# Performance work log

Measured on AMD Instinct MI355X. Metric: run time of the kernel, lower is better.

## Reference

```python
import jax, jax.numpy as jnp
import numpy as np

ATOM_F = 64
NBR_F = 64
IN_F = 2 * ATOM_F + NBR_F  # 192
ATTN = ATOM_F              # 64
ATTN_OUT = 4 * ATOM_F      # 256
EPS = 1e-5


def setup_inputs() -> dict:
    key = jax.random.key(0)
    ks = jax.random.split(key, 12)
    N, M = 65536, 12
    atom_in_fea = jax.random.normal(ks[0], (N, ATOM_F), dtype=jnp.float32)
    nbr_fea = jax.random.normal(ks[1], (N, M, NBR_F), dtype=jnp.float32)
    nbr_fea_idx = jax.random.randint(ks[2], (N, M), 0, N)
    s = 0.05
    WK = jax.random.normal(ks[3], (ATTN, IN_F), dtype=jnp.float32) * s
    WQ = jax.random.normal(ks[4], (ATTN, IN_F), dtype=jnp.float32) * s
    WV = jax.random.normal(ks[5], (ATTN, IN_F), dtype=jnp.float32) * s
    WO = jax.random.normal(ks[6], (ATTN_OUT, ATTN), dtype=jnp.float32) * s
    W_fc = jax.random.normal(ks[7], (2 * ATOM_F, ATTN_OUT), dtype=jnp.float32) * s
    b_fc = jax.random.normal(ks[8], (2 * ATOM_F,), dtype=jnp.float32) * s
    bn1_g = jnp.ones((2 * ATOM_F,), jnp.float32)
    bn1_b = jnp.zeros((2 * ATOM_F,), jnp.float32)
    bn2_g = jnp.ones((ATOM_F,), jnp.float32)
    bn2_b = jnp.zeros((ATOM_F,), jnp.float32)
    return {"atom_in_fea": atom_in_fea, "nbr_fea": nbr_fea, "nbr_fea_idx": nbr_fea_idx,
            "WK": WK, "WQ": WQ, "WV": WV, "WO": WO, "W_fc": W_fc, "b_fc": b_fc,
            "bn1_g": bn1_g, "bn1_b": bn1_b, "bn2_g": bn2_g, "bn2_b": bn2_b}


def _batchnorm(x2d, g, b):
    # training-mode BatchNorm1d: biased variance over the batch dim
    mean = jnp.mean(x2d, axis=0)
    var = jnp.mean((x2d - mean) ** 2, axis=0)
    return (x2d - mean) * jax.lax.rsqrt(var + EPS) * g + b


def reference(atom_in_fea, nbr_fea, nbr_fea_idx, WK, WQ, WV, WO,
              W_fc, b_fc, bn1_g, bn1_b, bn2_g, bn2_b):
    N, M = nbr_fea_idx.shape
    atom_nbr_fea = atom_in_fea[nbr_fea_idx]                       # (N, M, F)
    self_fea = jnp.broadcast_to(atom_in_fea[:, None, :], (N, M, ATOM_F))
    total = jnp.concatenate([self_fea, atom_nbr_fea, nbr_fea], axis=2)  # (N, M, 192)

    # self-attention over the M neighbor slots (dropout is identity at eval)
    K = jnp.einsum('nmf,af->nma', total, WK)
    Q = jnp.einsum('nmf,af->nma', total, WQ)
    V = jnp.einsum('nmf,af->nma', total, WV)
    logits = jnp.einsum('nma,nka->nmk', K, Q) / jnp.sqrt(jnp.float32(ATTN))
    w = jax.nn.softmax(logits, axis=-1)
    attn = jnp.einsum('nmk,nka->nma', w, V)                       # (N, M, 64)
    h = jnp.einsum('nma,oa->nmo', attn, WO)                       # (N, M, 256)

    gated = jnp.einsum('nmo,go->nmg', h, W_fc) + b_fc             # (N, M, 128)
    gated = _batchnorm(gated.reshape(-1, 2 * ATOM_F), bn1_g, bn1_b).reshape(N, M, 2 * ATOM_F)
    nbr_filter, nbr_core = jnp.split(gated, 2, axis=2)
    nbr_sumed = jnp.sum(jax.nn.sigmoid(nbr_filter) * jax.nn.softplus(nbr_core), axis=1)  # (N, 64)
    nbr_sumed = _batchnorm(nbr_sumed, bn2_g, bn2_b)
    return jax.nn.softplus(atom_in_fea + nbr_sumed)
```

## Files before the change

kernel.cpp:

```cpp
#include <hip/hip_runtime.h>
#include <stdint.h>


typedef unsigned short u16;
typedef __attribute__((ext_vector_type(8))) short short8;
typedef __attribute__((ext_vector_type(4))) short short4v;
typedef __attribute__((ext_vector_type(4))) float floatx4;

#define EPS 1e-5f
#define LOG2E 1.44269504f

#if defined(__has_builtin)
#if __has_builtin(__builtin_amdgcn_mfma_f32_16x16x16bf16_1k)
#define HAVE_M16 1
#endif
#endif
#ifndef HAVE_M16
#define HAVE_M16 0
#endif

#if HAVE_M16
#define VKW 20
#define WKW 20
#else
#define VKW 40
#define WKW 40
#endif

__device__ __forceinline__ u16 bf16r(float x) {
  uint32_t u = __float_as_uint(x);
  u = (u + 0x7fffu + ((u >> 16) & 1u)) >> 16;
  return (u16)u;
}
__device__ __forceinline__ float bf2f(u16 h) {
  return __uint_as_float(((uint32_t)h) << 16);
}
__device__ __forceinline__ uint32_t pkbf16(float a, float b) {
  union { __bf16 h[2]; uint32_t u; } r;
  r.h[0] = (__bf16)a; r.h[1] = (__bf16)b;
  return r.u;
}
__device__ __forceinline__ short8 pkfrag(float4 a, float4 b) {
  union { uint32_t u[4]; short8 s; } r;
  r.u[0] = pkbf16(a.x, a.y); r.u[1] = pkbf16(a.z, a.w);
  r.u[2] = pkbf16(b.x, b.y); r.u[3] = pkbf16(b.z, b.w);
  return r.s;
}
__device__ __forceinline__ float fexp(float x) { return __builtin_amdgcn_exp2f(x * LOG2E); }
__device__ __forceinline__ float frcp(float x) { return __builtin_amdgcn_rcpf(x); }
__device__ __forceinline__ float fsig(float x) { return frcp(1.0f + fexp(-x)); }
__device__ __forceinline__ float fsp(float x) {
  return fmaxf(x, 0.0f) + __builtin_amdgcn_logf(1.0f + fexp(-fabsf(x))) * 0.69314718f;
}

#define MFMA32(a, b, c) __builtin_amdgcn_mfma_f32_16x16x32_bf16((a), (b), (c), 0, 0, 0)

#define OFF_FRAGE 0
#define OFF_FRAGP 24576
#define OFF_FRAGC 73728
#define OFF_BN1S1 90112
#define OFF_BN1S2 221184
#define OFF_BN2S1 352256
#define OFF_BN2S2 417792
#define OFF_BNST  483328
#define OFF_NSUM  524288
#define OFF_P     17825792
#define OFF_ATTN  68157440

__global__ __launch_bounds__(256) void k_prep(
    const float* __restrict__ WK, const float* __restrict__ WQ, const float* __restrict__ WV,
    const float* __restrict__ WO, const float* __restrict__ Wfc,
    u16* __restrict__ fragE, u16* __restrict__ fragP, u16* __restrict__ fragC,
    float* __restrict__ zbase) {
  int b = blockIdx.x, t = threadIdx.x;
  if (b < 24) {
    int c = b >> 1, ks = b & 1;
    for (int e = t; e < 512; e += 256) {
      int l = e >> 3, j = e & 7;
      int col = c * 16 + (l & 15);
      int k = ks * 32 + ((l >> 4) & 3) * 8 + j;
      int which = col >> 6, a = col & 63;
      const float* W = (which == 0) ? WK : ((which == 1) ? WQ : WV);
      fragE[b * 512 + e] = bf16r(W[a * 192 + 128 + k]);
    }
  } else if (b < 72) {
    int tt = b - 24; int ks = tt & 1; int ct = tt >> 1;
    int part = ct / 12; int rem = ct % 12; int which = rem >> 2; int a16 = rem & 3;
    for (int e = t; e < 512; e += 256) {
      int l = e >> 3, j = e & 7;
      int a = a16 * 16 + (l & 15);
      int k = ks * 32 + ((l >> 4) & 3) * 8 + j;
      const float* W = (which == 0) ? WK : ((which == 1) ? WQ : WV);
      fragP[tt * 512 + e] = bf16r(W[a * 192 + part * 64 + k]);
    }
  } else if (b < 88) {
    int tile = b - 72;
    for (int e = t; e < 512; e += 256) {
      int l = e >> 3, j = e & 7;
      int g = (tile >> 1) * 16 + (l & 15);
      int a = (tile & 1) * 32 + ((l >> 4) & 3) * 8 + j;
      float acc = 0.f;
#pragma unroll 8
      for (int o = 0; o < 256; ++o) acc += Wfc[g * 256 + o] * WO[o * 64 + a];
      fragC[tile * 512 + e] = bf16r(acc);
    }
  } else {
    int idx = (b - 88) * 256 + t;
    if (idx < 98304) zbase[idx] = 0.f;
  }
}

__global__ __launch_bounds__(256) void k_proj(
    const float* __restrict__ atom_in, const u16* __restrict__ fragP,
    u16* __restrict__ P, int N) {
  int tid = threadIdx.x, lane = tid & 63, wid = tid >> 6;
  int rowbase = (blockIdx.x * 4 + wid) * 16;
  __shared__ __align__(16) u16 aA[4][16][72];
  for (int rr = 0; rr < 16; ++rr)
    aA[wid][rr][lane] = bf16r(atom_in[(size_t)(rowbase + rr) * 64 + lane]);
  int cl = lane & 15, q = lane >> 4;
  short8 a0 = *(const short8*)&aA[wid][cl][q * 8];
  short8 a1 = *(const short8*)&aA[wid][cl][32 + q * 8];
  for (int tile = 0; tile < 24; ++tile) {
    floatx4 acc = {0.f, 0.f, 0.f, 0.f};
    short8 b0 = *(const short8*)(fragP + (tile * 2 + 0) * 512 + lane * 8);
    short8 b1 = *(const short8*)(fragP + (tile * 2 + 1) * 512 + lane * 8);
    acc = MFMA32(a0, b0, acc);
    acc = MFMA32(a1, b1, acc);
    int part = tile / 12, rem = tile % 12;
    int which = rem >> 2, a16 = rem & 3;
    u16* Pm = P + (size_t)part * N * 192;
    uint32_t p01 = pkbf16(acc[0], acc[1]), p23 = pkbf16(acc[2], acc[3]);
    int nrow = rowbase + q * 4;
    uint32_t base = ((uint32_t)nrow * 3u + (uint32_t)which) * 64u + (uint32_t)cl * 4u + (uint32_t)a16;
    Pm[base]           = (u16)p01;
    Pm[base + 192u]    = (u16)(p01 >> 16);
    Pm[base + 384u]    = (u16)p23;
    Pm[base + 576u]    = (u16)(p23 >> 16);
  }
}

__global__ __launch_bounds__(256, 6) void k_main(
    const float* __restrict__ nbr_fea, const int* __restrict__ nbr_idx,
    const u16* __restrict__ P, const u16* __restrict__ fragE,
    const u16* __restrict__ fragC, const float* __restrict__ b_fc,
    u16* __restrict__ attn_out, float* __restrict__ bn1s1, float* __restrict__ bn1s2,
    int N) {
  int tid = threadIdx.x, lane = tid & 63, wid = tid >> 6;
  int n = blockIdx.x * 4 + wid;
  int cl = lane & 15, q = lane >> 4;

  __shared__ __align__(16) u16 KQ[4][16][72];
  __shared__ __align__(16) u16 Vt[4][64][VKW];
  union WU { u16 w[16][WKW]; float red[2][128]; };
  __shared__ __align__(16) WU WR[4];

  int4 gi = *(const int4*)(nbr_idx + (size_t)n * 12 + (q < 3 ? q : 2) * 4);
  int gv[4] = {gi.x, gi.y, gi.z, gi.w};

  short8 ea0, ea1;
  if (cl < 12) {
    const float* rp = nbr_fea + ((size_t)n * 12 + cl) * 64 + q * 8;
    float4 a0 = *(const float4*)rp;
    float4 a1 = *(const float4*)(rp + 4);
    float4 b0 = *(const float4*)(rp + 32);
    float4 b1 = *(const float4*)(rp + 36);
    ea0 = pkfrag(a0, a1);
    ea1 = pkfrag(b0, b1);
  } else {
#pragma unroll
    for (int j = 0; j < 8; ++j) { ea0[j] = 0; ea1[j] = 0; }
  }

  const char* Pself = (const char*)P;
  const char* Pnbrb = (const char*)(P + (size_t)N * 192);
  uint32_t cl8 = (uint32_t)cl * 8u;
  uint2 sW[3], nW[3][4];
  {
    uint32_t soff = (uint32_t)n * 384u + cl8;
#pragma unroll
    for (int w = 0; w < 3; ++w)
      sW[w] = *(const uint2*)(Pself + (soff + (uint32_t)w * 128u));
  }
#pragma unroll
  for (int w = 0; w < 3; ++w)
#pragma unroll
    for (int r = 0; r < 4; ++r)
      nW[w][r] = *(const uint2*)(Pnbrb + ((uint32_t)gv[r] * 384u + (uint32_t)w * 128u + cl8));

#if HAVE_M16
  *(uint32_t*)&Vt[wid][lane][12] = 0u;
  *(uint32_t*)&Vt[wid][lane][14] = 0u;
#else
#pragma unroll
  for (int kk = 12; kk < 32; kk += 2) *(uint32_t*)&Vt[wid][lane][kk] = 0u;
#endif

#define STAGE1_TILE(c, which)                                                 \
  {                                                                           \
    floatx4 acc = {0.f, 0.f, 0.f, 0.f};                                       \
    short8 b0 = *(const short8*)(fragE + ((c) * 2 + 0) * 512 + lane * 8);     \
    short8 b1 = *(const short8*)(fragE + ((c) * 2 + 1) * 512 + lane * 8);     \
    acc = MFMA32(ea0, b0, acc);                                               \
    acc = MFMA32(ea1, b1, acc);                                               \
    int colb = ((c) & 3) * 16 + cl;                                           \
    const u16* sp = (const u16*)&sW[(which)];                                 \
    float ps = bf2f(sp[(c) & 3]);                                             \
    float v0 = acc[0] + ps + bf2f(((const u16*)&nW[(which)][0])[(c) & 3]);    \
    float v1 = acc[1] + ps + bf2f(((const u16*)&nW[(which)][1])[(c) & 3]);    \
    float v2 = acc[2] + ps + bf2f(((const u16*)&nW[(which)][2])[(c) & 3]);    \
    float v3 = acc[3] + ps + bf2f(((const u16*)&nW[(which)][3])[(c) & 3]);    \
    uint32_t p01 = pkbf16(v0, v1), p23 = pkbf16(v2, v3);                      \
    if ((which) < 2) {                                                        \
      KQ[wid][q * 4 + 0][colb] = (u16)p01;                                    \
      KQ[wid][q * 4 + 1][colb] = (u16)(p01 >> 16);                            \
      KQ[wid][q * 4 + 2][colb] = (u16)p23;                                    \
      KQ[wid][q * 4 + 3][colb] = (u16)(p23 >> 16);                            \
    } else if (q < 3) {                                                       \
      *(uint2*)&Vt[wid][colb][q * 4] = make_uint2(p01, p23);                  \
    }                                                                         \
  }

#pragma unroll
  for (int c = 0; c < 4; ++c) STAGE1_TILE(c, 0)
  short8 ka0 = *(const short8*)&KQ[wid][cl][q * 8];
  short8 ka1 = *(const short8*)&KQ[wid][cl][32 + q * 8];
#pragma unroll
  for (int c = 4; c < 8; ++c) STAGE1_TILE(c, 1)
  short8 qb0 = *(const short8*)&KQ[wid][cl][q * 8];
  short8 qb1 = *(const short8*)&KQ[wid][cl][32 + q * 8];
#pragma unroll
  for (int c = 8; c < 12; ++c) STAGE1_TILE(c, 2)

  floatx4 lacc = {0.f, 0.f, 0.f, 0.f};
  lacc = MFMA32(ka0, qb0, lacc);
  lacc = MFMA32(ka1, qb1, lacc);

  float w4[4];
#pragma unroll
  for (int r = 0; r < 4; ++r) {
    float e = (cl < 12) ? fexp(lacc[r] * 0.125f) : 0.f;
    float s = e;
    s += __shfl_xor(s, 1); s += __shfl_xor(s, 2);
    s += __shfl_xor(s, 4); s += __shfl_xor(s, 8);
    w4[r] = e * frcp(s);
  }
  {
    uint32_t p01 = pkbf16(w4[0], w4[1]), p23 = pkbf16(w4[2], w4[3]);
    WR[wid].w[q * 4 + 0][cl] = (u16)p01;
    WR[wid].w[q * 4 + 1][cl] = (u16)(p01 >> 16);
    WR[wid].w[q * 4 + 2][cl] = (u16)p23;
    WR[wid].w[q * 4 + 3][cl] = (u16)(p23 >> 16);
  }
#if !HAVE_M16
  for (int i = lane; i < 128; i += 64) {
    int rr = i >> 3, cc = 16 + ((i & 7) << 1);
    *(uint32_t*)&WR[wid].w[rr][cc] = 0u;
  }
#endif

#if HAVE_M16
  short4v wa = *(const short4v*)&WR[wid].w[cl][q * 4];
#pragma unroll
  for (int c = 0; c < 4; ++c) {
    floatx4 acc = {0.f, 0.f, 0.f, 0.f};
    short4v vb = *(const short4v*)&Vt[wid][c * 16 + cl][q * 4];
    acc = __builtin_amdgcn_mfma_f32_16x16x16bf16_1k(wa, vb, acc, 0, 0, 0);
    uint32_t p01 = pkbf16(acc[0], acc[1]), p23 = pkbf16(acc[2], acc[3]);
    KQ[wid][q * 4 + 0][c * 16 + cl] = (u16)p01;
    KQ[wid][q * 4 + 1][c * 16 + cl] = (u16)(p01 >> 16);
    KQ[wid][q * 4 + 2][c * 16 + cl] = (u16)p23;
    KQ[wid][q * 4 + 3][c * 16 + cl] = (u16)(p23 >> 16);
  }
#else
  short8 wa = *(const short8*)&WR[wid].w[cl][q * 8];
#pragma unroll
  for (int c = 0; c < 4; ++c) {
    floatx4 acc = {0.f, 0.f, 0.f, 0.f};
    short8 vb = *(const short8*)&Vt[wid][c * 16 + cl][q * 8];
    acc = MFMA32(wa, vb, acc);
    uint32_t p01 = pkbf16(acc[0], acc[1]), p23 = pkbf16(acc[2], acc[3]);
    KQ[wid][q * 4 + 0][c * 16 + cl] = (u16)p01;
    KQ[wid][q * 4 + 1][c * 16 + cl] = (u16)(p01 >> 16);
    KQ[wid][q * 4 + 2][c * 16 + cl] = (u16)p23;
    KQ[wid][q * 4 + 3][c * 16 + cl] = (u16)(p23 >> 16);
  }
#endif

  {
    char* ab = (char*)attn_out + (uint32_t)n * 1536u;
#pragma unroll
    for (int i = 0; i < 3; ++i) {
      int j = i * 64 + lane;
      uint2 d = *(const uint2*)&KQ[wid][j >> 4][(j & 15) * 4];
      *(uint2*)(ab + ((uint32_t)(j >> 4) * 128u + (uint32_t)(j & 15) * 8u)) = d;
    }
  }

  short8 aa0 = *(const short8*)&KQ[wid][cl][q * 8];
  short8 aa1 = *(const short8*)&KQ[wid][cl][32 + q * 8];
  float regA[8], regB[8];
#pragma unroll
  for (int c = 0; c < 8; ++c) {
    floatx4 acc = {0.f, 0.f, 0.f, 0.f};
    short8 b0 = *(const short8*)(fragC + (c * 2 + 0) * 512 + lane * 8);
    short8 b1 = *(const short8*)(fragC + (c * 2 + 1) * 512 + lane * 8);
    acc = MFMA32(aa0, b0, acc);
    acc = MFMA32(aa1, b1, acc);
    float bias = b_fc[c * 16 + cl];
    float s1 = 0.f, s2 = 0.f;
    if (q < 3) {
#pragma unroll
      for (int r = 0; r < 4; ++r) {
        float v = acc[r] + bias;
        s1 += v; s2 += v * v;
      }
    }
    s1 += __shfl_xor(s1, 16); s1 += __shfl_xor(s1, 32);
    s2 += __shfl_xor(s2, 16); s2 += __shfl_xor(s2, 32);
    regA[c] = s1; regB[c] = s2;
  }
  if (lane < 16) {
#pragma unroll
    for (int c = 0; c < 8; ++c) {
      WR[wid].red[0][c * 16 + cl] = regA[c];
      WR[wid].red[1][c * 16 + cl] = regB[c];
    }
  }
  __syncthreads();
  if (tid < 128) {
    float a1 = WR[0].red[0][tid] + WR[1].red[0][tid] + WR[2].red[0][tid] + WR[3].red[0][tid];
    float a2 = WR[0].red[1][tid] + WR[1].red[1][tid] + WR[2].red[1][tid] + WR[3].red[1][tid];
    int rep = blockIdx.x & 255;
    atomicAdd(&bn1s1[rep * 128 + tid], a1);
    atomicAdd(&bn1s2[rep * 128 + tid], a2);
  }
}

__global__ __launch_bounds__(1024) void k_bn1(
    const float* __restrict__ bn1s1, const float* __restrict__ bn1s2,
    const float* __restrict__ g1, const float* __restrict__ b1,
    const float* __restrict__ bfc, float* __restrict__ bnst, float count) {
  int t = threadIdx.x;
  int f = t & 127, chunk = t >> 7;
  float s1 = 0.f, s2 = 0.f;
  for (int r = chunk * 32; r < chunk * 32 + 32; ++r) {
    s1 += bn1s1[r * 128 + f]; s2 += bn1s2[r * 128 + f];
  }
  __shared__ float p1[1024], p2[1024];
  p1[t] = s1; p2[t] = s2;
  __syncthreads();
  if (t < 128) {
    s1 = 0.f; s2 = 0.f;
#pragma unroll
    for (int k = 0; k < 8; ++k) { s1 += p1[t + 128 * k]; s2 += p2[t + 128 * k]; }
    float mean = s1 / count;
    float var = s2 / count - mean * mean;
    float sc = g1[t] * rsqrtf(var + EPS);
    bnst[t] = sc;
    bnst[128 + t] = (bfc[t] - mean) * sc + b1[t];
  }
}

__global__ __launch_bounds__(256) void k_gate(
    const u16* __restrict__ attn, const u16* __restrict__ fragC,
    const float* __restrict__ bnst,
    float* __restrict__ ns, float* __restrict__ bn2s1, float* __restrict__ bn2s2, int N) {
  int tid = threadIdx.x, lane = tid & 63, wid = tid >> 6;
  int n = blockIdx.x * 4 + wid;
  int cl = lane & 15, q = lane >> 4;
  __shared__ float scS[128], shS[128];
  __shared__ float r1[4][64], r2[4][64];
  if (tid < 128) scS[tid] = bnst[tid];
  else           shS[tid - 128] = bnst[tid];
  __syncthreads();

  short8 aa0, aa1;
  if (cl < 12) {
    const char* rp = (const char*)attn + ((uint32_t)n * 1536u + (uint32_t)cl * 128u);
    aa0 = *(const short8*)(rp + q * 16);
    aa1 = *(const short8*)(rp + 64 + q * 16);
  } else {
#pragma unroll
    for (int j = 0; j < 8; ++j) { aa0[j] = 0; aa1[j] = 0; }
  }

  floatx4 acc[8];
#pragma unroll
  for (int c = 0; c < 8; ++c) {
    floatx4 z = {0.f, 0.f, 0.f, 0.f};
    short8 b0 = *(const short8*)(fragC + (c * 2 + 0) * 512 + lane * 8);
    short8 b1 = *(const short8*)(fragC + (c * 2 + 1) * 512 + lane * 8);
    z = MFMA32(aa0, b0, z);
    acc[c] = MFMA32(aa1, b1, z);
  }

  float s[4];
#pragma unroll
  for (int c = 0; c < 4; ++c) {
    int gF = c * 16 + cl, gC = gF + 64;
    float scf = scS[gF], shf = shS[gF], scc = scS[gC], shc = shS[gC];
    float sum = 0.f;
    if (q < 3) {
#pragma unroll
      for (int r = 0; r < 4; ++r) {
        float xf = acc[c][r] * scf + shf;
        float xc = acc[c + 4][r] * scc + shc;
        sum += fsig(xf) * fsp(xc);
      }
    }
    sum += __shfl_xor(sum, 16);
    sum += __shfl_xor(sum, 32);
    s[c] = sum;
  }
  if (lane < 16) {
#pragma unroll
    for (int c = 0; c < 4; ++c) {
      ns[(size_t)n * 64 + c * 16 + cl] = s[c];
      r1[wid][c * 16 + cl] = s[c];
      r2[wid][c * 16 + cl] = s[c] * s[c];
    }
  }
  __syncthreads();
  if (tid < 64) {
    float a1 = r1[0][tid] + r1[1][tid] + r1[2][tid] + r1[3][tid];
    float a2 = r2[0][tid] + r2[1][tid] + r2[2][tid] + r2[3][tid];
    int rep = blockIdx.x & 255;
    atomicAdd(&bn2s1[rep * 64 + tid], a1);
    atomicAdd(&bn2s2[rep * 64 + tid], a2);
  }
}

__global__ __launch_bounds__(512) void k_bn2(
    const float* __restrict__ bn2s1, const float* __restrict__ bn2s2,
    const float* __restrict__ g2, const float* __restrict__ b2,
    float* __restrict__ bnst, float count) {
  int t = threadIdx.x;
  int f = t & 63, part = t >> 6;
  float s1 = 0.f, s2 = 0.f;
  for (int r = part * 32; r < part * 32 + 32; ++r) {
    s1 += bn2s1[r * 64 + f]; s2 += bn2s2[r * 64 + f];
  }
  __shared__ float p1[512], p2[512];
  p1[t] = s1; p2[t] = s2;
  __syncthreads();
  if (t < 64) {
    s1 = 0.f; s2 = 0.f;
#pragma unroll
    for (int k = 0; k < 8; ++k) { s1 += p1[t + 64 * k]; s2 += p2[t + 64 * k]; }
    float mean = s1 / count;
    float var = s2 / count - mean * mean;
    float sc = g2[t] * rsqrtf(var + EPS);
    bnst[256 + t] = sc;
    bnst[320 + t] = b2[t] - mean * sc;
  }
}

__global__ __launch_bounds__(256) void k_out(
    const float* __restrict__ atom_in, const float* __restrict__ ns,
    const float* __restrict__ bnst, float* __restrict__ out, int total) {
  int i = blockIdx.x * 256 + threadIdx.x;
  if (i < total) {
    int f = i & 63;
    float v = atom_in[i] + ns[i] * bnst[256 + f] + bnst[320 + f];
    out[i] = fsp(v);
  }
}

extern "C" void kernel_launch(void* const* d_in, const int* in_sizes, int n_in,
                              void* d_out, int out_size, void* d_ws, size_t ws_size,
                              hipStream_t stream) {
  const float* atom_in = (const float*)d_in[0];
  const float* nbr_fea = (const float*)d_in[1];
  const int*   nbr_idx = (const int*)d_in[2];
  const float* WK  = (const float*)d_in[3];
  const float* WQ  = (const float*)d_in[4];
  const float* WV  = (const float*)d_in[5];
  const float* WO  = (const float*)d_in[6];
  const float* Wfc = (const float*)d_in[7];
  const float* bfc = (const float*)d_in[8];
  const float* g1  = (const float*)d_in[9];
  const float* b1  = (const float*)d_in[10];
  const float* g2  = (const float*)d_in[11];
  const float* b2  = (const float*)d_in[12];
  int N = in_sizes[0] / 64;

  char* ws = (char*)d_ws;
  u16*   fragE = (u16*)(ws + OFF_FRAGE);
  u16*   fragP = (u16*)(ws + OFF_FRAGP);
  u16*   fragC = (u16*)(ws + OFF_FRAGC);
  float* bn1s1 = (float*)(ws + OFF_BN1S1);
  float* bn1s2 = (float*)(ws + OFF_BN1S2);
  float* bn2s1 = (float*)(ws + OFF_BN2S1);
  float* bn2s2 = (float*)(ws + OFF_BN2S2);
  float* bnst  = (float*)(ws + OFF_BNST);
  float* nsum  = (float*)(ws + OFF_NSUM);
  u16*   P     = (u16*)(ws + OFF_P);
  u16*   attn  = (u16*)(ws + OFF_ATTN);
  float* out   = (float*)d_out;

  hipLaunchKernelGGL(k_prep, dim3(472), dim3(256), 0, stream,
                     WK, WQ, WV, WO, Wfc, fragE, fragP, fragC, bn1s1);
  hipLaunchKernelGGL(k_proj, dim3(N / 64), dim3(256), 0, stream, atom_in, fragP, P, N);
  hipLaunchKernelGGL(k_main, dim3(N / 4), dim3(256), 0, stream,
                     nbr_fea, nbr_idx, P, fragE, fragC, bfc, attn, bn1s1, bn1s2, N);
  hipLaunchKernelGGL(k_bn1, dim3(1), dim3(1024), 0, stream,
                     bn1s1, bn1s2, g1, b1, bfc, bnst, (float)(N * 12));
  hipLaunchKernelGGL(k_gate, dim3(N / 4), dim3(256), 0, stream,
                     attn, fragC, bnst, nsum, bn2s1, bn2s2, N);
  hipLaunchKernelGGL(k_bn2, dim3(1), dim3(512), 0, stream,
                     bn2s1, bn2s2, g2, b2, bnst, (float)N);
  hipLaunchKernelGGL(k_out, dim3((N * 64) / 256), dim3(256), 0, stream,
                     atom_in, nsum, bnst, out, N * 64);
}
```

Measured before the change: 587.9 us.

## Stage WO in shared memory for prep, alias KQ buffer, raise main occupancy

The fused Wfc·WO weight product in k_prep now stages WO through shared memory in two halves and has each thread accumulate two outputs, which should make that prep path cheaper. In k_main the KQ scratch buffer is merged into the existing per-wave union so it shares LDS with the weight and reduction buffers. The launch bound's minimum-blocks hint rises from 6 to 8 to allow more resident waves, at the risk of register spills. k_gate copies fragC into LDS once per block instead of having every wave read it from global/L2.

```diff
diff --git a/kernel.cpp b/kernel.cpp
--- a/kernel.cpp
+++ b/kernel.cpp
@@ -72,6 +72,7 @@
     const float* __restrict__ WO, const float* __restrict__ Wfc,
     u16* __restrict__ fragE, u16* __restrict__ fragP, u16* __restrict__ fragC,
     float* __restrict__ zbase) {
+  __shared__ float woS[128 * 64];
   int b = blockIdx.x, t = threadIdx.x;
   if (b < 24) {
     int c = b >> 1, ks = b & 1;
@@ -95,15 +96,26 @@
     }
   } else if (b < 88) {
     int tile = b - 72;
-    for (int e = t; e < 512; e += 256) {
-      int l = e >> 3, j = e & 7;
-      int g = (tile >> 1) * 16 + (l & 15);
-      int a = (tile & 1) * 32 + ((l >> 4) & 3) * 8 + j;
-      float acc = 0.f;
+    float acc0 = 0.f, acc1 = 0.f;
+    for (int half = 0; half < 2; ++half) {
+      __syncthreads();
+      for (int i = t; i < 8192; i += 256) woS[i] = WO[half * 8192 + i];
+      __syncthreads();
+#pragma unroll
+      for (int e2 = 0; e2 < 2; ++e2) {
+        int e = e2 * 256 + t;
+        int l = e >> 3, j = e & 7;
+        int g = (tile >> 1) * 16 + (l & 15);
+        int a = (tile & 1) * 32 + ((l >> 4) & 3) * 8 + j;
+        float s = (e2 == 0) ? acc0 : acc1;
+        const float* wr = Wfc + g * 256 + half * 128;
 #pragma unroll 8
-      for (int o = 0; o < 256; ++o) acc += Wfc[g * 256 + o] * WO[o * 64 + a];
-      fragC[tile * 512 + e] = bf16r(acc);
-    }
+        for (int o = 0; o < 128; ++o) s += wr[o] * woS[o * 64 + a];
+        if (e2 == 0) acc0 = s; else acc1 = s;
+      }
+    }
+    fragC[tile * 512 + t]       = bf16r(acc0);
+    fragC[tile * 512 + 256 + t] = bf16r(acc1);
   } else {
     int idx = (b - 88) * 256 + t;
     if (idx < 98304) zbase[idx] = 0.f;
@@ -140,7 +152,7 @@
   }
 }
 
-__global__ __launch_bounds__(256, 6) void k_main(
+__global__ __launch_bounds__(256, 8) void k_main(
     const float* __restrict__ nbr_fea, const int* __restrict__ nbr_idx,
     const u16* __restrict__ P, const u16* __restrict__ fragE,
     const u16* __restrict__ fragC, const float* __restrict__ b_fc,
@@ -150,10 +162,13 @@
   int n = blockIdx.x * 4 + wid;
   int cl = lane & 15, q = lane >> 4;
 
-  __shared__ __align__(16) u16 KQ[4][16][72];
+  union WU {
+    u16 kq[16][72];
+    u16 w[16][WKW];
+    float red[2][128];
+  };
+  __shared__ __align__(16) WU WR[4];
   __shared__ __align__(16) u16 Vt[4][64][VKW];
-  union WU { u16 w[16][WKW]; float red[2][128]; };
-  __shared__ __align__(16) WU WR[4];
 
   int4 gi = *(const int4*)(nbr_idx + (size_t)n * 12 + (q < 3 ? q : 2) * 4);
   int gv[4] = {gi.x, gi.y, gi.z, gi.w};
@@ -212,10 +227,10 @@
     float v3 = acc[3] + ps + bf2f(((const u16*)&nW[(which)][3])[(c) & 3]);    \
     uint32_t p01 = pkbf16(v0, v1), p23 = pkbf16(v2, v3);                      \
     if ((which) < 2) {                                                        \
-      KQ[wid][q * 4 + 0][colb] = (u16)p01;                                    \
-      KQ[wid][q * 4 + 1][colb] = (u16)(p01 >> 16);                            \
-      KQ[wid][q * 4 + 2][colb] = (u16)p23;                                    \
-      KQ[wid][q * 4 + 3][colb] = (u16)(p23 >> 16);                            \
+      WR[wid].kq[q * 4 + 0][colb] = (u16)p01;                                 \
+      WR[wid].kq[q * 4 + 1][colb] = (u16)(p01 >> 16);                         \
+      WR[wid].kq[q * 4 + 2][colb] = (u16)p23;                                 \
+      WR[wid].kq[q * 4 + 3][colb] = (u16)(p23 >> 16);                         \
     } else if (q < 3) {                                                       \
       *(uint2*)&Vt[wid][colb][q * 4] = make_uint2(p01, p23);                  \
     }                                                                         \
@@ -223,12 +238,12 @@
 
 #pragma unroll
   for (int c = 0; c < 4; ++c) STAGE1_TILE(c, 0)
-  short8 ka0 = *(const short8*)&KQ[wid][cl][q * 8];
-  short8 ka1 = *(const short8*)&KQ[wid][cl][32 + q * 8];
+  short8 ka0 = *(const short8*)&WR[wid].kq[cl][q * 8];
+  short8 ka1 = *(const short8*)&WR[wid].kq[cl][32 + q * 8];
 #pragma unroll
   for (int c = 4; c < 8; ++c) STAGE1_TILE(c, 1)
-  short8 qb0 = *(const short8*)&KQ[wid][cl][q * 8];
-  short8 qb1 = *(const short8*)&KQ[wid][cl][32 + q * 8];
+  short8 qb0 = *(const short8*)&WR[wid].kq[cl][q * 8];
+  short8 qb1 = *(const short8*)&WR[wid].kq[cl][32 + q * 8];
 #pragma unroll
   for (int c = 8; c < 12; ++c) STAGE1_TILE(c, 2)
 
@@ -267,10 +282,10 @@
     short4v vb = *(const short4v*)&Vt[wid][c * 16 + cl][q * 4];
     acc = __builtin_amdgcn_mfma_f32_16x16x16bf16_1k(wa, vb, acc, 0, 0, 0);
     uint32_t p01 = pkbf16(acc[0], acc[1]), p23 = pkbf16(acc[2], acc[3]);
-    KQ[wid][q * 4 + 0][c * 16 + cl] = (u16)p01;
-    KQ[wid][q * 4 + 1][c * 16 + cl] = (u16)(p01 >> 16);
-    KQ[wid][q * 4 + 2][c * 16 + cl] = (u16)p23;
-    KQ[wid][q * 4 + 3][c * 16 + cl] = (u16)(p23 >> 16);
+    WR[wid].kq[q * 4 + 0][c * 16 + cl] = (u16)p01;
+    WR[wid].kq[q * 4 + 1][c * 16 + cl] = (u16)(p01 >> 16);
+    WR[wid].kq[q * 4 + 2][c * 16 + cl] = (u16)p23;
+    WR[wid].kq[q * 4 + 3][c * 16 + cl] = (u16)(p23 >> 16);
   }
 #else
   short8 wa = *(const short8*)&WR[wid].w[cl][q * 8];
@@ -280,10 +295,10 @@
     short8 vb = *(const short8*)&Vt[wid][c * 16 + cl][q * 8];
     acc = MFMA32(wa, vb, acc);
     uint32_t p01 = pkbf16(acc[0], acc[1]), p23 = pkbf16(acc[2], acc[3]);
-    KQ[wid][q * 4 + 0][c * 16 + cl] = (u16)p01;
-    KQ[wid][q * 4 + 1][c * 16 + cl] = (u16)(p01 >> 16);
-    KQ[wid][q * 4 + 2][c * 16 + cl] = (u16)p23;
-    KQ[wid][q * 4 + 3][c * 16 + cl] = (u16)(p23 >> 16);
+    WR[wid].kq[q * 4 + 0][c * 16 + cl] = (u16)p01;
+    WR[wid].kq[q * 4 + 1][c * 16 + cl] = (u16)(p01 >> 16);
+    WR[wid].kq[q * 4 + 2][c * 16 + cl] = (u16)p23;
+    WR[wid].kq[q * 4 + 3][c * 16 + cl] = (u16)(p23 >> 16);
   }
 #endif
 
@@ -292,13 +307,13 @@
 #pragma unroll
     for (int i = 0; i < 3; ++i) {
       int j = i * 64 + lane;
-      uint2 d = *(const uint2*)&KQ[wid][j >> 4][(j & 15) * 4];
+      uint2 d = *(const uint2*)&WR[wid].kq[j >> 4][(j & 15) * 4];
       *(uint2*)(ab + ((uint32_t)(j >> 4) * 128u + (uint32_t)(j & 15) * 8u)) = d;
     }
   }
 
-  short8 aa0 = *(const short8*)&KQ[wid][cl][q * 8];
-  short8 aa1 = *(const short8*)&KQ[wid][cl][32 + q * 8];
+  short8 aa0 = *(const short8*)&WR[wid].kq[cl][q * 8];
+  short8 aa1 = *(const short8*)&WR[wid].kq[cl][32 + q * 8];
   float regA[8], regB[8];
 #pragma unroll
   for (int c = 0; c < 8; ++c) {
@@ -369,10 +384,13 @@
   int tid = threadIdx.x, lane = tid & 63, wid = tid >> 6;
   int n = blockIdx.x * 4 + wid;
   int cl = lane & 15, q = lane >> 4;
+  __shared__ __align__(16) u16 fCs[8192];
   __shared__ float scS[128], shS[128];
   __shared__ float r1[4][64], r2[4][64];
   if (tid < 128) scS[tid] = bnst[tid];
   else           shS[tid - 128] = bnst[tid];
+  for (int i = tid; i < 1024; i += 256)
+    ((uint4*)fCs)[i] = ((const uint4*)fragC)[i];
   __syncthreads();
 
   short8 aa0, aa1;
@@ -389,8 +407,8 @@
 #pragma unroll
   for (int c = 0; c < 8; ++c) {
     floatx4 z = {0.f, 0.f, 0.f, 0.f};
-    short8 b0 = *(const short8*)(fragC + (c * 2 + 0) * 512 + lane * 8);
-    short8 b1 = *(const short8*)(fragC + (c * 2 + 1) * 512 + lane * 8);
+    short8 b0 = *(const short8*)(fCs + (c * 2 + 0) * 512 + lane * 8);
+    short8 b1 = *(const short8*)(fCs + (c * 2 + 1) * 512 + lane * 8);
     z = MFMA32(aa0, b0, z);
     acc[c] = MFMA32(aa1, b1, z);
   }
```

Result: faster. 537.4 us (-8.6%).
